# Kernel tuning notes

Measured on AMD Instinct MI355X. Metric: run time of the kernel, lower is better.

Reference implementation:

```python
import jax, jax.numpy as jnp
import numpy as np

# irreps: 4096x0e + 4096x1o + 4096x2e + 4096x3o (in == out)
MULS = [4096, 4096, 4096, 4096]
DIMS = [1, 3, 5, 7]  # 2l+1 for l = 0,1,2,3

def _build_paths():
    paths = []
    off = 0
    w_ptr = 0
    for mul, d in zip(MULS, DIMS):
        # (input offset, mul_in, ir dim, weight offset, mul_out)
        paths.append((off, mul, d, w_ptr, mul))
        off += mul * d
        w_ptr += mul * mul
    return paths

PATHS = _build_paths()
DIM_TOT = sum(m * d for m, d in zip(MULS, DIMS))  # 65536
W_TOT = sum(m * m for m in MULS)                  # 67108864


def setup_inputs() -> dict:
    key = jax.random.key(0)
    k1, k2 = jax.random.split(key)
    inp = jax.random.normal(k1, (DIM_TOT,), dtype=jnp.float32)
    weights = jax.random.normal(k2, (W_TOT,), dtype=jnp.float32)
    return {"input": inp, "weights": weights}


def reference(input, weights):
    chunks = []
    for off, mul_in, d, w_off, mul_out in PATHS:
        chunk_in = input[off:off + mul_in * d].reshape(mul_in, d)
        w = weights[w_off:w_off + mul_in * mul_out].reshape(mul_in, mul_out)
        norm = np.float32(np.sqrt(1.0 / mul_in))
        # 'ui,uv->vi' then ravel: output is (mul_out, d) flattened
        chunk_out = jnp.einsum('ui,uv->vi', chunk_in, w).reshape(-1) * norm
        chunks.append(chunk_out)
    return jnp.concatenate(chunks)
```

## Files before the change

kernel.cpp:

```cpp
#include <hip/hip_runtime.h>
#include <stdint.h>


constexpr int MUL = 4096;
constexpr int VT  = 64;
constexpr int NQ  = 16;
constexpr int SC  = 4;
constexpr int SCU = MUL / SC;
constexpr int UPT = SCU / NQ;
constexpr int PF  = 16;

template<int D>
__device__ __forceinline__ void body(
    const float* __restrict__ w, const float* __restrict__ x,
    float* __restrict__ out, float* xs, float* red,
    int io_off, long w_off, int v0)
{
  const int t  = threadIdx.x;
  const int lv = t & 63;
  const int q  = t >> 6;
  const long wcol = w_off + v0 + lv;

  float acc[D];
  #pragma unroll
  for (int i = 0; i < D; ++i) acc[i] = 0.f;

  for (int c = 0; c < SC; ++c) {
    const int ub = c * SCU;
    __syncthreads();
    for (int j = t; j < SCU * D; j += 1024)
      xs[j] = x[io_off + ub * D + j];
    __syncthreads();

    const int u0 = q * UPT;
    for (int bb = 0; bb < UPT; bb += PF) {
      float wv[PF];
      #pragma unroll
      for (int j = 0; j < PF; ++j)
        wv[j] = w[wcol + (long)(ub + u0 + bb + j) * MUL];
      #pragma unroll
      for (int j = 0; j < PF; ++j) {
        const float* xr = xs + (u0 + bb + j) * D;
        #pragma unroll
        for (int i = 0; i < D; ++i)
          acc[i] = fmaf(wv[j], xr[i], acc[i]);
      }
    }
  }

  #pragma unroll
  for (int i = 0; i < D; ++i)
    red[q * VT * D + lv * D + i] = acc[i];
  __syncthreads();

  for (int j = t; j < VT * D; j += 1024) {
    float s = 0.f;
    #pragma unroll
    for (int qq = 0; qq < NQ; ++qq) s += red[qq * VT * D + j];
    out[io_off + v0 * D + j] = s * 0.015625f;
  }
}

__global__ __launch_bounds__(1024)
void linear_all(const float* __restrict__ w, const float* __restrict__ x,
                float* __restrict__ out)
{
  __shared__ float xs [SCU * 7];
  __shared__ float red[NQ * VT * 7];
  const int b  = blockIdx.x;
  const int p  = b >> 6;
  const int v0 = (b & 63) * VT;

  if      (p == 0) body<1>(w, x, out, xs, red,     0,         0L, v0);
  else if (p == 1) body<3>(w, x, out, xs, red,  4096, 16777216L, v0);
  else if (p == 2) body<5>(w, x, out, xs, red, 16384, 33554432L, v0);
  else             body<7>(w, x, out, xs, red, 36864, 50331648L, v0);
}

extern "C" void kernel_launch(void* const* d_in, const int* in_sizes, int n_in,
                              void* d_out, int out_size, void* d_ws, size_t ws_size,
                              hipStream_t stream) {
  const float* x = (const float*)d_in[0];
  const float* w = (const float*)d_in[1];
  linear_all<<<256, 1024, 0, stream>>>(w, x, (float*)d_out);
}
```

Measured before the change: 357.9 us.

## Split reduction dimension across blocks with float4 weight loads and two-pass reduce

```diff
diff --git a/kernel.cpp b/kernel.cpp
--- a/kernel.cpp
+++ b/kernel.cpp
@@ -3,78 +3,148 @@
 
 
 constexpr int MUL = 4096;
-constexpr int VT  = 64;
-constexpr int NQ  = 16;
-constexpr int SC  = 4;
-constexpr int SCU = MUL / SC;
-constexpr int UPT = SCU / NQ;
-constexpr int PF  = 16;
+constexpr int UC_ROWS = 64;
+
 
 template<int D>
-__device__ __forceinline__ void body(
+__device__ __forceinline__ void p1body(
     const float* __restrict__ w, const float* __restrict__ x,
-    float* __restrict__ out, float* xs, float* red,
-    int io_off, long w_off, int v0)
+    float* __restrict__ part, int io_off, long w_off, long pbase, int uc)
 {
-  const int t  = threadIdx.x;
-  const int lv = t & 63;
-  const int q  = t >> 6;
-  const long wcol = w_off + v0 + lv;
+  const int t = threadIdx.x;
+  const float* __restrict__ wp = w + w_off + (long)uc * (UC_ROWS * (long)MUL) + (t << 2);
+  const float* __restrict__ xg = x + io_off + uc * (UC_ROWS * D);
 
-  float acc[D];
+  float acc[D][4];
   #pragma unroll
-  for (int i = 0; i < D; ++i) acc[i] = 0.f;
+  for (int i = 0; i < D; ++i) {
+    #pragma unroll
+    for (int j = 0; j < 4; ++j) acc[i][j] = 0.f;
+  }
 
-  for (int c = 0; c < SC; ++c) {
-    const int ub = c * SCU;
-    __syncthreads();
-    for (int j = t; j < SCU * D; j += 1024)
-      xs[j] = x[io_off + ub * D + j];
-    __syncthreads();
-
-    const int u0 = q * UPT;
-    for (int bb = 0; bb < UPT; bb += PF) {
-      float wv[PF];
+  for (int u0 = 0; u0 < UC_ROWS; u0 += 8) {
+    float4 wv[8];
+    #pragma unroll
+    for (int j = 0; j < 8; ++j)
+      wv[j] = *reinterpret_cast<const float4*>(wp + (long)(u0 + j) * MUL);
+    #pragma unroll
+    for (int j = 0; j < 8; ++j) {
       #pragma unroll
-      for (int j = 0; j < PF; ++j)
-        wv[j] = w[wcol + (long)(ub + u0 + bb + j) * MUL];
-      #pragma unroll
-      for (int j = 0; j < PF; ++j) {
-        const float* xr = xs + (u0 + bb + j) * D;
-        #pragma unroll
-        for (int i = 0; i < D; ++i)
-          acc[i] = fmaf(wv[j], xr[i], acc[i]);
+      for (int i = 0; i < D; ++i) {
+        const float xv = xg[(u0 + j) * D + i];
+        acc[i][0] = fmaf(wv[j].x, xv, acc[i][0]);
+        acc[i][1] = fmaf(wv[j].y, xv, acc[i][1]);
+        acc[i][2] = fmaf(wv[j].z, xv, acc[i][2]);
+        acc[i][3] = fmaf(wv[j].w, xv, acc[i][3]);
       }
     }
   }
 
+  alignas(16) float tmp[4 * D];
   #pragma unroll
-  for (int i = 0; i < D; ++i)
-    red[q * VT * D + lv * D + i] = acc[i];
-  __syncthreads();
+  for (int j = 0; j < 4; ++j) {
+    #pragma unroll
+    for (int i = 0; i < D; ++i) tmp[j * D + i] = acc[i][j];
+  }
+  float4* dst = reinterpret_cast<float4*>(
+      part + pbase + (long)uc * (MUL * (long)D) + (long)(t * 4) * D);
+  #pragma unroll
+  for (int m = 0; m < D; ++m)
+    dst[m] = reinterpret_cast<const float4*>(tmp)[m];
+}
 
-  for (int j = t; j < VT * D; j += 1024) {
-    float s = 0.f;
+__global__ __launch_bounds__(1024)
+void linear_p1(const float* __restrict__ w, const float* __restrict__ x,
+               float* __restrict__ part)
+{
+  const int b  = blockIdx.x;
+  const int p  = b >> 6;
+  const int uc = b & 63;
+  if      (p == 0) p1body<1>(w, x, part,     0,         0L,       0L, uc);
+  else if (p == 1) p1body<3>(w, x, part,  4096,  16777216L,  262144L, uc);
+  else if (p == 2) p1body<5>(w, x, part, 16384,  33554432L, 1048576L, uc);
+  else             p1body<7>(w, x, part, 36864,  50331648L, 2359296L, uc);
+}
+
+template<int D>
+__device__ __forceinline__ void p2body(
+    const float* __restrict__ part, float* __restrict__ out,
+    int io_off, long pbase, int oblk)
+{
+  const int o = oblk * 256 + threadIdx.x;
+  const float* __restrict__ q = part + pbase + o;
+  float s0 = 0.f, s1 = 0.f, s2 = 0.f, s3 = 0.f;
+  #pragma unroll
+  for (int u = 0; u < 64; u += 4) {
+    s0 += q[(long)(u + 0) * (MUL * D)];
+    s1 += q[(long)(u + 1) * (MUL * D)];
+    s2 += q[(long)(u + 2) * (MUL * D)];
+    s3 += q[(long)(u + 3) * (MUL * D)];
+  }
+  out[io_off + o] = ((s0 + s1) + (s2 + s3)) * 0.015625f;
+}
+
+__global__ __launch_bounds__(256)
+void linear_p2(const float* __restrict__ part, float* __restrict__ out)
+{
+  const int b = blockIdx.x;
+  if      (b < 16)  p2body<1>(part, out,     0,       0L, b);
+  else if (b < 64)  p2body<3>(part, out,  4096,  262144L, b - 16);
+  else if (b < 144) p2body<5>(part, out, 16384, 1048576L, b - 64);
+  else              p2body<7>(part, out, 36864, 2359296L, b - 144);
+}
+
+template<int D>
+__device__ __forceinline__ void p1abody(
+    const float* __restrict__ w, const float* __restrict__ x,
+    float* __restrict__ out, int io_off, long w_off, int uc)
+{
+  const int t = threadIdx.x;
+  const float* __restrict__ wp = w + w_off + (long)uc * (UC_ROWS * (long)MUL) + (t << 2);
+  const float* __restrict__ xg = x + io_off + uc * (UC_ROWS * D);
+
+  float acc[D][4];
+  #pragma unroll
+  for (int i = 0; i < D; ++i) {
     #pragma unroll
-    for (int qq = 0; qq < NQ; ++qq) s += red[qq * VT * D + j];
-    out[io_off + v0 * D + j] = s * 0.015625f;
+    for (int j = 0; j < 4; ++j) acc[i][j] = 0.f;
+  }
+  for (int u0 = 0; u0 < UC_ROWS; u0 += 8) {
+    float4 wv[8];
+    #pragma unroll
+    for (int j = 0; j < 8; ++j)
+      wv[j] = *reinterpret_cast<const float4*>(wp + (long)(u0 + j) * MUL);
+    #pragma unroll
+    for (int j = 0; j < 8; ++j) {
+      #pragma unroll
+      for (int i = 0; i < D; ++i) {
+        const float xv = xg[(u0 + j) * D + i];
+        acc[i][0] = fmaf(wv[j].x, xv, acc[i][0]);
+        acc[i][1] = fmaf(wv[j].y, xv, acc[i][1]);
+        acc[i][2] = fmaf(wv[j].z, xv, acc[i][2]);
+        acc[i][3] = fmaf(wv[j].w, xv, acc[i][3]);
+      }
+    }
+  }
+  #pragma unroll
+  for (int j = 0; j < 4; ++j) {
+    #pragma unroll
+    for (int i = 0; i < D; ++i)
+      atomicAdd(out + io_off + (t * 4 + j) * D + i, acc[i][j] * 0.015625f);
   }
 }
 
 __global__ __launch_bounds__(1024)
-void linear_all(const float* __restrict__ w, const float* __restrict__ x,
-                float* __restrict__ out)
+void linear_p1_atomic(const float* __restrict__ w, const float* __restrict__ x,
+                      float* __restrict__ out)
 {
-  __shared__ float xs [SCU * 7];
-  __shared__ float red[NQ * VT * 7];
   const int b  = blockIdx.x;
   const int p  = b >> 6;
-  const int v0 = (b & 63) * VT;
-
-  if      (p == 0) body<1>(w, x, out, xs, red,     0,         0L, v0);
-  else if (p == 1) body<3>(w, x, out, xs, red,  4096, 16777216L, v0);
-  else if (p == 2) body<5>(w, x, out, xs, red, 16384, 33554432L, v0);
-  else             body<7>(w, x, out, xs, red, 36864, 50331648L, v0);
+  const int uc = b & 63;
+  if      (p == 0) p1abody<1>(w, x, out,     0,         0L, uc);
+  else if (p == 1) p1abody<3>(w, x, out,  4096,  16777216L, uc);
+  else if (p == 2) p1abody<5>(w, x, out, 16384,  33554432L, uc);
+  else             p1abody<7>(w, x, out, 36864,  50331648L, uc);
 }
 
 extern "C" void kernel_launch(void* const* d_in, const int* in_sizes, int n_in,
@@ -82,5 +152,13 @@
                               hipStream_t stream) {
   const float* x = (const float*)d_in[0];
   const float* w = (const float*)d_in[1];
-  linear_all<<<256, 1024, 0, stream>>>(w, x, (float*)d_out);
+  const size_t need = 4194304UL * sizeof(float);
+  if (d_ws != nullptr && ws_size >= need) {
+    float* part = (float*)d_ws;
+    linear_p1<<<256, 1024, 0, stream>>>(w, x, part);
+    linear_p2<<<256, 256, 0, stream>>>(part, (float*)d_out);
+  } else {
+    hipMemsetAsync(d_out, 0, 65536 * sizeof(float), stream);
+    linear_p1_atomic<<<256, 1024, 0, stream>>>(w, x, (float*)d_out);
+  }
 }
```

New measurement: 365.3 us. 2.1% more time.

## Split-K over 16 chunks with atomics and wide float4 weight loads

Applied to the files above, without the earlier changes.

```diff
diff --git a/kernel.cpp b/kernel.cpp
--- a/kernel.cpp
+++ b/kernel.cpp
@@ -3,78 +3,82 @@
 
 
 constexpr int MUL = 4096;
-constexpr int VT  = 64;
-constexpr int NQ  = 16;
-constexpr int SC  = 4;
-constexpr int SCU = MUL / SC;
-constexpr int UPT = SCU / NQ;
-constexpr int PF  = 16;
+
 
 template<int D>
 __device__ __forceinline__ void body(
     const float* __restrict__ w, const float* __restrict__ x,
-    float* __restrict__ out, float* xs, float* red,
-    int io_off, long w_off, int v0)
+    float* __restrict__ out, float* __restrict__ xs,
+    int io_off, long w_off, int b128)
 {
-  const int t  = threadIdx.x;
-  const int lv = t & 63;
-  const int q  = t >> 6;
-  const long wcol = w_off + v0 + lv;
+  const int t   = threadIdx.x;
+  const int vg  = t & 63;
+  const int q   = t >> 6;
+  const int vt  = b128 >> 4;
+  const int uc  = b128 & 15;
+  const int v0  = vt * 512 + vg * 8;
+  const int u0g = uc * 256;
 
-  float acc[D];
+  for (int j = t; j < 256 * D; j += 512)
+    xs[j] = x[io_off + u0g * D + j];
+  __syncthreads();
+
+  const float* __restrict__ wp = w + w_off + (long)u0g * MUL + v0;
+
+  float acc[D][8];
   #pragma unroll
-  for (int i = 0; i < D; ++i) acc[i] = 0.f;
+  for (int i = 0; i < D; ++i) {
+    #pragma unroll
+    for (int j = 0; j < 8; ++j) acc[i][j] = 0.f;
+  }
 
-  for (int c = 0; c < SC; ++c) {
-    const int ub = c * SCU;
-    __syncthreads();
-    for (int j = t; j < SCU * D; j += 1024)
-      xs[j] = x[io_off + ub * D + j];
-    __syncthreads();
-
-    const int u0 = q * UPT;
-    for (int bb = 0; bb < UPT; bb += PF) {
-      float wv[PF];
+  const int ub0 = q * 32;
+  for (int ub = 0; ub < 32; ub += 4) {
+    float4 wa[4], wb[4];
+    #pragma unroll
+    for (int k = 0; k < 4; ++k) {
+      const float* p = wp + (long)(ub0 + ub + k) * MUL;
+      wa[k] = *reinterpret_cast<const float4*>(p);
+      wb[k] = *reinterpret_cast<const float4*>(p + 4);
+    }
+    #pragma unroll
+    for (int k = 0; k < 4; ++k) {
       #pragma unroll
-      for (int j = 0; j < PF; ++j)
-        wv[j] = w[wcol + (long)(ub + u0 + bb + j) * MUL];
-      #pragma unroll
-      for (int j = 0; j < PF; ++j) {
-        const float* xr = xs + (u0 + bb + j) * D;
-        #pragma unroll
-        for (int i = 0; i < D; ++i)
-          acc[i] = fmaf(wv[j], xr[i], acc[i]);
+      for (int i = 0; i < D; ++i) {
+        const float xv = xs[(ub0 + ub + k) * D + i];
+        acc[i][0] = fmaf(wa[k].x, xv, acc[i][0]);
+        acc[i][1] = fmaf(wa[k].y, xv, acc[i][1]);
+        acc[i][2] = fmaf(wa[k].z, xv, acc[i][2]);
+        acc[i][3] = fmaf(wa[k].w, xv, acc[i][3]);
+        acc[i][4] = fmaf(wb[k].x, xv, acc[i][4]);
+        acc[i][5] = fmaf(wb[k].y, xv, acc[i][5]);
+        acc[i][6] = fmaf(wb[k].z, xv, acc[i][6]);
+        acc[i][7] = fmaf(wb[k].w, xv, acc[i][7]);
       }
     }
   }
 
   #pragma unroll
-  for (int i = 0; i < D; ++i)
-    red[q * VT * D + lv * D + i] = acc[i];
-  __syncthreads();
-
-  for (int j = t; j < VT * D; j += 1024) {
-    float s = 0.f;
+  for (int j = 0; j < 8; ++j) {
     #pragma unroll
-    for (int qq = 0; qq < NQ; ++qq) s += red[qq * VT * D + j];
-    out[io_off + v0 * D + j] = s * 0.015625f;
+    for (int i = 0; i < D; ++i)
+      atomicAdd(out + io_off + (long)(v0 + j) * D + i, acc[i][j] * 0.015625f);
   }
 }
 
-__global__ __launch_bounds__(1024)
-void linear_all(const float* __restrict__ w, const float* __restrict__ x,
-                float* __restrict__ out)
+__global__ __launch_bounds__(512)
+void linear_fused(const float* __restrict__ w, const float* __restrict__ x,
+                  float* __restrict__ out)
 {
-  __shared__ float xs [SCU * 7];
-  __shared__ float red[NQ * VT * 7];
-  const int b  = blockIdx.x;
-  const int p  = b >> 6;
-  const int v0 = (b & 63) * VT;
+  __shared__ float xs[256 * 7];
+  const int b    = blockIdx.x;
+  const int p    = b >> 7;
+  const int b128 = b & 127;
 
-  if      (p == 0) body<1>(w, x, out, xs, red,     0,         0L, v0);
-  else if (p == 1) body<3>(w, x, out, xs, red,  4096, 16777216L, v0);
-  else if (p == 2) body<5>(w, x, out, xs, red, 16384, 33554432L, v0);
-  else             body<7>(w, x, out, xs, red, 36864, 50331648L, v0);
+  if      (p == 0) body<1>(w, x, out, xs,     0,         0L, b128);
+  else if (p == 1) body<3>(w, x, out, xs,  4096,  16777216L, b128);
+  else if (p == 2) body<5>(w, x, out, xs, 16384,  33554432L, b128);
+  else             body<7>(w, x, out, xs, 36864,  50331648L, b128);
 }
 
 extern "C" void kernel_launch(void* const* d_in, const int* in_sizes, int n_in,
@@ -82,5 +86,6 @@
                               hipStream_t stream) {
   const float* x = (const float*)d_in[0];
   const float* w = (const float*)d_in[1];
-  linear_all<<<256, 1024, 0, stream>>>(w, x, (float*)d_out);
+  hipMemsetAsync(d_out, 0, out_size, stream);
+  linear_fused<<<512, 512, 0, stream>>>(w, x, (float*)d_out);
 }
```

Result: slower. 722.4 us (+101.9%).

## Vectorize weight loads as float4 per lane with wave-shuffle partial reduction

Applied to the files above, without the earlier changes.

```diff
diff --git a/kernel.cpp b/kernel.cpp
--- a/kernel.cpp
+++ b/kernel.cpp
@@ -3,78 +3,101 @@
 
 
 constexpr int MUL = 4096;
-constexpr int VT  = 64;
-constexpr int NQ  = 16;
-constexpr int SC  = 4;
-constexpr int SCU = MUL / SC;
-constexpr int UPT = SCU / NQ;
-constexpr int PF  = 16;
 
 template<int D>
 __device__ __forceinline__ void body(
     const float* __restrict__ w, const float* __restrict__ x,
-    float* __restrict__ out, float* xs, float* red,
+    float* __restrict__ out, float* __restrict__ xs, float* __restrict__ red,
     int io_off, long w_off, int v0)
 {
   const int t  = threadIdx.x;
-  const int lv = t & 63;
+  const int l  = t & 63;
   const int q  = t >> 6;
-  const long wcol = w_off + v0 + lv;
+  const int cg = l & 15;
+  const int rs = l >> 4;
 
-  float acc[D];
+  const float* __restrict__ wp = w + w_off + v0 + (cg << 2);
+
+  float acc[D][4];
   #pragma unroll
-  for (int i = 0; i < D; ++i) acc[i] = 0.f;
+  for (int i = 0; i < D; ++i) {
+    #pragma unroll
+    for (int j = 0; j < 4; ++j) acc[i][j] = 0.f;
+  }
 
-  for (int c = 0; c < SC; ++c) {
-    const int ub = c * SCU;
+  for (int sc = 0; sc < 4; ++sc) {
     __syncthreads();
-    for (int j = t; j < SCU * D; j += 1024)
-      xs[j] = x[io_off + ub * D + j];
+    #pragma unroll
+    for (int j = 0; j < D; ++j)
+      xs[t + j * 1024] = x[io_off + sc * 1024 * D + t + j * 1024];
     __syncthreads();
 
-    const int u0 = q * UPT;
-    for (int bb = 0; bb < UPT; bb += PF) {
-      float wv[PF];
+    const int rbase = q * 64;
+    for (int bb = 0; bb < 16; bb += 8) {
+      float4 wv[8];
       #pragma unroll
-      for (int j = 0; j < PF; ++j)
-        wv[j] = w[wcol + (long)(ub + u0 + bb + j) * MUL];
+      for (int k = 0; k < 8; ++k) {
+        const int r = rbase + ((bb + k) << 2) + rs;
+        wv[k] = *reinterpret_cast<const float4*>(
+            wp + (long)(sc * 1024 + r) * MUL);
+      }
       #pragma unroll
-      for (int j = 0; j < PF; ++j) {
-        const float* xr = xs + (u0 + bb + j) * D;
+      for (int k = 0; k < 8; ++k) {
+        const int r = rbase + ((bb + k) << 2) + rs;
+        const float* xr = xs + r * D;
         #pragma unroll
-        for (int i = 0; i < D; ++i)
-          acc[i] = fmaf(wv[j], xr[i], acc[i]);
+        for (int i = 0; i < D; ++i) {
+          acc[i][0] = fmaf(wv[k].x, xr[i], acc[i][0]);
+          acc[i][1] = fmaf(wv[k].y, xr[i], acc[i][1]);
+          acc[i][2] = fmaf(wv[k].z, xr[i], acc[i][2]);
+          acc[i][3] = fmaf(wv[k].w, xr[i], acc[i][3]);
+        }
       }
     }
   }
 
   #pragma unroll
-  for (int i = 0; i < D; ++i)
-    red[q * VT * D + lv * D + i] = acc[i];
+  for (int i = 0; i < D; ++i) {
+    #pragma unroll
+    for (int j = 0; j < 4; ++j) {
+      acc[i][j] += __shfl_xor(acc[i][j], 16);
+      acc[i][j] += __shfl_xor(acc[i][j], 32);
+    }
+  }
+
+  __syncthreads();
+  if (rs == 0) {
+    #pragma unroll
+    for (int j = 0; j < 4; ++j) {
+      #pragma unroll
+      for (int i = 0; i < D; ++i)
+        red[(q * 64 + (cg << 2) + j) * D + i] = acc[i][j];
+    }
+  }
   __syncthreads();
 
-  for (int j = t; j < VT * D; j += 1024) {
+  for (int o = t; o < 64 * D; o += 1024) {
     float s = 0.f;
     #pragma unroll
-    for (int qq = 0; qq < NQ; ++qq) s += red[qq * VT * D + j];
-    out[io_off + v0 * D + j] = s * 0.015625f;
+    for (int qq = 0; qq < 16; ++qq) s += red[qq * 64 * D + o];
+    out[io_off + v0 * D + o] = s * 0.015625f;
   }
 }
 
-__global__ __launch_bounds__(1024)
+__global__ __launch_bounds__(1024, 4)
 void linear_all(const float* __restrict__ w, const float* __restrict__ x,
                 float* __restrict__ out)
 {
-  __shared__ float xs [SCU * 7];
-  __shared__ float red[NQ * VT * 7];
+  __shared__ float xs [1024 * 7];
+  __shared__ float red[16 * 64 * 7];
   const int b  = blockIdx.x;
   const int p  = b >> 6;
-  const int v0 = (b & 63) * VT;
+  const int v0 = (b & 63) * 64;
 
   if      (p == 0) body<1>(w, x, out, xs, red,     0,         0L, v0);
-  else if (p == 1) body<3>(w, x, out, xs, red,  4096, 16777216L, v0);
-  else if (p == 2) body<5>(w, x, out, xs, red, 16384, 33554432L, v0);
-  else             body<7>(w, x, out, xs, red, 36864, 50331648L, v0);
+  else if (p == 1) body<3>(w, x, out, xs, red,  4096,  16777216L, v0);
+  else if (p == 2) body<5>(w, x, out, xs, red, 16384,  33554432L, v0);
+  else             body<7>(w, x, out, xs, red, 36864,  50331648L, v0);
 }
 
 extern "C" void kernel_launch(void* const* d_in, const int* in_sizes, int n_in,
```

After: 364.5 us. About the same (+1.9%).
